# Kernel tuning notes

Measured on AMD Instinct MI355X. Metric: run time of the kernel, lower is better.

## Reference

```python
import jax, jax.numpy as jnp
import numpy as np

N, E, G, L, H, TD, F = 10000, 100000, 64, 2, 512, 256, 128
DIS = 2 * 3 * F            # sinusoid embedding dim = 768
DIN = 2 * H + DIS + 6      # edge_mlp input dim = 1798
EPS = 1e-5


def _ln(x, g, b):
    mu = x.mean(-1, keepdims=True)
    var = ((x - mu) ** 2).mean(-1, keepdims=True)
    return (x - mu) * jax.lax.rsqrt(var + EPS) * g + b


def _sin_emb(x):  # x: [E, 3] -> [E, 2*3*F]
    freqs = 2.0 * np.pi * jnp.arange(F, dtype=x.dtype)
    e = (x[:, :, None] * freqs).reshape(x.shape[0], -1)
    return jnp.concatenate([jnp.sin(e), jnp.cos(e)], axis=-1)


def setup_inputs() -> dict:
    key = jax.random.key(0)
    ks = jax.random.split(key, 16)
    s = 0.02
    return dict(
        atom_types=jax.random.randint(ks[0], (N,), 0, 100),
        node2graph=jnp.sort(jax.random.randint(ks[1], (N,), 0, G)),
        edge_index=jax.random.randint(ks[2], (2, E), 0, N),
        frac_diff=jax.random.uniform(ks[3], (E, 3)) - 0.5,
        lattices=jax.random.normal(ks[4], (G, 6)),
        t=jax.random.uniform(ks[5], (1, 1)),
        emb_table=jax.random.normal(ks[6], (119, H)) * s,
        Wt=jax.random.normal(ks[7], (TD, 1)) * s,
        Wa=jax.random.normal(ks[8], (H, H + TD)) * s,
        ba=jnp.zeros((H,)),
        ln_g=jnp.ones((L, H)), ln_b=jnp.zeros((L, H)),
        eW1=jax.random.normal(ks[9], (L, H, DIN)) * s, eb1=jnp.zeros((L, H)),
        eW2=jax.random.normal(ks[10], (L, H, H)) * s, eb2=jnp.zeros((L, H)),
        nW1=jax.random.normal(ks[11], (L, H, 2 * H)) * s, nb1=jnp.zeros((L, H)),
        nW2=jax.random.normal(ks[12], (L, H, H)) * s, nb2=jnp.zeros((L, H)),
        fln_g=jnp.ones((H,)), fln_b=jnp.zeros((H,)),
        Wc=jax.random.normal(ks[13], (3, H)) * s,
    )


def reference(atom_types, node2graph, edge_index, frac_diff, lattices, t,
              emb_table, Wt, Wa, ba, ln_g, ln_b, eW1, eb1, eW2, eb2,
              nW1, nb1, nW2, nb2, fln_g, fln_b, Wc):
    silu = jax.nn.silu
    src, dst = edge_index[0], edge_index[1]
    edge2graph = node2graph[src]
    demb = _sin_emb(frac_diff)                 # [E, 768]
    lat_e = lattices[edge2graph]               # [E, 6] (lattices_flat gathered to edges)
    counts = jax.ops.segment_sum(jnp.ones((E, 1), frac_diff.dtype), src, num_segments=N)
    counts = jnp.maximum(counts, 1.0)

    # node init: embedding + broadcast time emb -> atom_latent_emb -> silu
    t_emb = t @ Wt.T                           # [1, TD]
    h = jnp.concatenate([emb_table[atom_types],
                         jnp.broadcast_to(t_emb, (N, TD))], axis=1)
    h = silu(h @ Wa.T + ba)                    # [N, H]

    def step(h, p):
        g, b, w1, b1, w2, b2, m1, c1, m2, c2 = p
        hn = _ln(h, g, b)                      # pre-LN
        ef = jnp.concatenate([hn[src], hn[dst], lat_e, demb], axis=1)  # [E, DIN]
        m = silu(ef @ w1.T + b1)
        m = silu(m @ w2.T + b2)                # [E, H] edge messages
        agg = jax.ops.segment_sum(m, src, num_segments=N) / counts    # scatter-mean
        u = jnp.concatenate([hn, agg], axis=1)  # [N, 2H]
        u = silu(u @ m1.T + c1)
        u = silu(u @ m2.T + c2)
        return h + u, None                     # residual

    h, _ = jax.lax.scan(step, h, (ln_g, ln_b, eW1, eb1, eW2, eb2,
                                  nW1, nb1, nW2, nb2))
    h = _ln(h, fln_g, fln_b)
    return h @ Wc.T                            # [N, 3] coord_out
```

## Files before the change

### kernel.cpp

```cpp
#include <hip/hip_runtime.h>
#include <stdint.h>

typedef unsigned short u16;
typedef unsigned int u32;
typedef __attribute__((ext_vector_type(8))) short short8;
typedef __attribute__((ext_vector_type(4))) float f32x4;

#define TN 10000
#define TE 100000
#define TG 64
#define TH 512
#define EC 25000
#define NCH 4
#define PAD 128

static constexpr size_t A256(size_t x){ return (x+255)/256*256; }
constexpr size_t OFF_H    = 0;
constexpr size_t OFF_PQ   = A256(OFF_H    + (size_t)TN*512*4);
constexpr size_t OFF_HCAT = A256(OFF_PQ   + (size_t)TN*1024*2);
constexpr size_t OFF_AGGF = A256(OFF_HCAT + (size_t)TN*1024*2);
constexpr size_t OFF_MC   = A256(OFF_AGGF + (size_t)TN*512*4);
constexpr size_t OFF_XD   = A256(OFF_MC   + (size_t)(EC+PAD)*512*2);
constexpr size_t OFF_WAB  = A256(OFF_XD   + (size_t)(EC+PAD)*768*2);
constexpr size_t OFF_W1D  = A256(OFF_WAB  + (size_t)2*1024*512*2);
constexpr size_t OFF_W2   = A256(OFF_W1D  + (size_t)2*512*768*2);
constexpr size_t OFF_WN1  = A256(OFF_W2   + (size_t)2*512*512*2);
constexpr size_t OFF_WN2  = A256(OFF_WN1  + (size_t)2*512*1024*2);
constexpr size_t OFF_RP   = A256(OFF_WN2  + (size_t)2*512*512*2);
constexpr size_t OFF_H0   = A256(OFF_RP   + (size_t)2*64*512*4);
constexpr size_t OFF_B2   = A256(OFF_H0   + (size_t)119*512*4);
constexpr size_t OFF_CNT  = A256(OFF_B2   + 512*4);
constexpr size_t OFF_SLOT = A256(OFF_CNT  + (size_t)TN*4);
constexpr size_t OFF_IPTR = A256(OFF_SLOT + (size_t)TN*4);
constexpr size_t OFF_NOD  = A256(OFF_IPTR + (size_t)(TN+1)*4);
constexpr size_t OFF_DST  = A256(OFF_NOD  + (size_t)(TE+PAD)*4);
constexpr size_t OFF_FDS  = A256(OFF_DST  + (size_t)(TE+PAD)*4);
constexpr size_t WS_NEED  = OFF_FDS + (size_t)(TE+PAD)*3*4;

__device__ __forceinline__ float bf2f(u16 u){ u32 x=((u32)u)<<16; float f; __builtin_memcpy(&f,&x,4); return f; }
__device__ __forceinline__ u16 f2bf(float f){ u32 x; __builtin_memcpy(&x,&f,4); x = x + 0x7fffu + ((x>>16)&1u); return (u16)(x>>16); }
__device__ __forceinline__ float siluf(float v){ return v*(1.0f/(1.0f+__expf(-v))); }

__device__ __forceinline__ void gld16(const void* g, void* l){
  __builtin_amdgcn_global_load_lds((const __attribute__((address_space(1))) u32*)g,
                                   (__attribute__((address_space(3))) u32*)l, 16, 0, 0);
}

__device__ __forceinline__ void blockReduce2(float& s, float& ss){
  for (int off=32; off>0; off>>=1){ s += __shfl_down(s,off,64); ss += __shfl_down(ss,off,64); }
  __shared__ float red[8];
  int lane = threadIdx.x&63, wave = threadIdx.x>>6;
  if (lane==0){ red[wave*2]=s; red[wave*2+1]=ss; }
  __syncthreads();
  s  = red[0]+red[2]+red[4]+red[6];
  ss = red[1]+red[3]+red[5]+red[7];
}

template<int EPI>
__device__ __forceinline__ void gemm_core(
    const u16* __restrict__ A, int lda,
    const u16* __restrict__ B, int ldb,
    int M, int K,
    u16* __restrict__ Cb, float* __restrict__ Cf, int ldc,
    const float* __restrict__ bias,
    int cbase,
    const u16* __restrict__ PQ,
    const int* __restrict__ nodS, const int* __restrict__ dstS,
    const int* __restrict__ n2g, const float* __restrict__ Rp)
{
  __shared__ u16 As[3*2048];
  __shared__ u16 Bs[3*4096];
  const int t = threadIdx.x;
  const int bm = blockIdx.x, bn = blockIdx.y;
  const int lane = t&63;
  const int wave = t>>6;
  const int wm = wave>>1, wn = wave&1;

  f32x4 acc[2][4];
  #pragma unroll
  for (int i=0;i<2;i++)
    #pragma unroll
    for (int j=0;j<4;j++) acc[i][j] = (f32x4){0.f,0.f,0.f,0.f};

  const int sr = t>>2;
  const int sk = (((t&3) ^ ((t>>3)&3)))*8;
  int ar0 = bm*64 + sr; if (ar0 > M-1) ar0 = M-1;
  const u16* Ag0 = A + (size_t)ar0*lda + sk;
  const u16* Bg0 = B + (size_t)(bn*128 + sr)*ldb + sk;
  const u16* Bg1 = B + (size_t)(bn*128 + sr + 64)*ldb + sk;
  u16* As0 = &As[t*8];
  u16* Bs0 = &Bs[t*8];
  u16* Bs1 = &Bs[t*8 + 2048];

  const int rg = ((lane>>4) ^ ((lane>>1)&3))*8;
  const u16* ApL = &As[(wm*32 + (lane&15))*32 + rg];
  const u16* BpL = &Bs[(wn*64 + (lane&15))*32 + rg];

  const int nk = K>>5;
  #define STAGE(kt, b) { const int ko=(kt)<<5; \
      gld16(Ag0+ko, As0+(b)*2048); \
      gld16(Bg0+ko, Bs0+(b)*4096); \
      gld16(Bg1+ko, Bs1+(b)*4096); }

  STAGE(0,0)
  STAGE(1,1)
  int cb=0, sb=2;
  for (int ki=0; ki<nk; ++ki){
    if (ki+1 < nk) asm volatile("s_waitcnt vmcnt(3)" ::: "memory");
    else           asm volatile("s_waitcnt vmcnt(0)" ::: "memory");
    __builtin_amdgcn_s_barrier();
    if (ki+2 < nk) STAGE(ki+2, sb)
    const int ca = cb*2048, cbb = cb*4096;
    short8 af[2], bf[4];
    #pragma unroll
    for (int mi=0;mi<2;mi++) af[mi] = *(const short8*)(ApL + ca + mi*512);
    #pragma unroll
    for (int ni=0;ni<4;ni++) bf[ni] = *(const short8*)(BpL + cbb + ni*512);
    #pragma unroll
    for (int mi=0;mi<2;mi++)
      #pragma unroll
      for (int ni=0;ni<4;ni++)
        acc[mi][ni] = __builtin_amdgcn_mfma_f32_16x16x32_bf16(af[mi], bf[ni], acc[mi][ni], 0,0,0);
    cb = (cb==2)?0:cb+1;
    sb = (sb==2)?0:sb+1;
  }
  #undef STAGE

  const int c0 = bn*128 + wn*64 + (lane&15);
  const int r0 = bm*64 + wm*32 + ((lane>>4)<<2);

  if constexpr (EPI==0){
    #pragma unroll
    for (int mi=0;mi<2;mi++)
      #pragma unroll
      for (int r=0;r<4;r++){
        int row = r0 + mi*16 + r;
        if (row < M){
          u16* o = Cb + (size_t)row*ldc + c0;
          #pragma unroll
          for (int ni=0;ni<4;ni++) o[ni*16] = f2bf(acc[mi][ni][r]);
        }
      }
  } else if constexpr (EPI==1){
    float bz[4];
    #pragma unroll
    for (int ni=0;ni<4;ni++) bz[ni] = bias[c0 + ni*16];
    #pragma unroll
    for (int mi=0;mi<2;mi++)
      #pragma unroll
      for (int r=0;r<4;r++){
        int row = r0 + mi*16 + r;
        if (row < M){
          u16* o = Cb + (size_t)row*ldc + c0;
          #pragma unroll
          for (int ni=0;ni<4;ni++) o[ni*16] = f2bf(siluf(acc[mi][ni][r]+bz[ni]));
        }
      }
  } else if constexpr (EPI==2){
    #pragma unroll
    for (int mi=0;mi<2;mi++)
      #pragma unroll
      for (int r=0;r<4;r++){
        int row = r0 + mi*16 + r;
        if (row < M){
          int gs = cbase + row;
          int sn = nodS[gs], dn = dstS[gs];
          int g  = n2g[sn];
          const u16* Pp = PQ + (size_t)sn*1024 + c0;
          const u16* Qp = PQ + (size_t)dn*1024 + 512 + c0;
          const float* Rr = Rp + g*512 + c0;
          u16* o = Cb + (size_t)row*512 + c0;
          #pragma unroll
          for (int ni=0;ni<4;ni++){
            float v = acc[mi][ni][r] + bf2f(Pp[ni*16]) + bf2f(Qp[ni*16]) + Rr[ni*16];
            o[ni*16] = f2bf(siluf(v));
          }
        }
      }
  } else {
    float bz[4];
    #pragma unroll
    for (int ni=0;ni<4;ni++) bz[ni] = bias[c0 + ni*16];
    #pragma unroll
    for (int mi=0;mi<2;mi++)
      #pragma unroll
      for (int r=0;r<4;r++){
        int row = r0 + mi*16 + r;
        if (row < M){
          float* hp = Cf + (size_t)row*ldc + c0;
          #pragma unroll
          for (int ni=0;ni<4;ni++) hp[ni*16] += siluf(acc[mi][ni][r]+bz[ni]);
        }
      }
  }
}

#define GEMM_ARGS const u16* A, int lda, const u16* B, int ldb, int M, int K, \
    u16* Cb, float* Cf, int ldc, const float* bias, int cbase, const u16* PQ, \
    const int* nodS, const int* dstS, const int* n2g, const float* Rp
#define GEMM_PASS A,lda,B,ldb,M,K,Cb,Cf,ldc,bias,cbase,PQ,nodS,dstS,n2g,Rp

__global__ __launch_bounds__(256) void g_pq(GEMM_ARGS){ gemm_core<0>(GEMM_PASS); }
__global__ __launch_bounds__(256) void g_e1(GEMM_ARGS){ gemm_core<2>(GEMM_PASS); }
__global__ __launch_bounds__(256) void g_e2(GEMM_ARGS){ gemm_core<1>(GEMM_PASS); }
__global__ __launch_bounds__(256) void g_n1(GEMM_ARGS){ gemm_core<1>(GEMM_PASS); }
__global__ __launch_bounds__(256) void g_n2(GEMM_ARGS){ gemm_core<3>(GEMM_PASS); }

__global__ void k_demb(const float* __restrict__ fdS, int cbase, int M,
                       u16* __restrict__ dembC){
  const float TP = 6.283185307179586f;
  int total = M*96;
  for (int i = blockIdx.x*blockDim.x+threadIdx.x; i<total; i+=gridDim.x*blockDim.x){
    int row = i/96;
    int g   = i - row*96;
    int col = g*8;
    int iscos = col>=384;
    int cc = iscos ? col-384 : col;
    int d = cc>>7;
    float off = iscos ? 0.25f : 0.0f;
    float x = fdS[(size_t)(cbase+row)*3 + d];
    float fb = (float)(cc&127);
    short8 v;
    #pragma unroll
    for (int j=0;j<8;j++){
      float w = x*(fb+(float)j);
      w -= rintf(w);
      v[j] = (short)f2bf(__sinf(TP*(w+off)));
    }
    *(short8*)(dembC + (size_t)row*768 + col) = v;
  }
}

__global__ void k_prep(const float* __restrict__ tp, const float* __restrict__ Wt,
                       const float* __restrict__ Wa, const float* __restrict__ ba,
                       float* __restrict__ bias2){
  __shared__ float te[256];
  int t=threadIdx.x;
  te[t] = tp[0]*Wt[t];
  __syncthreads();
  for (int i=t;i<512;i+=256){
    float s = ba[i];
    const float* wr = Wa + (size_t)i*768 + 512;
    for (int j=0;j<256;j++) s += wr[j]*te[j];
    bias2[i]=s;
  }
}

__global__ void k_h0(const float* __restrict__ emb, const float* __restrict__ Wa,
                     const float* __restrict__ bias2, float* __restrict__ h0){
  __shared__ float et[512];
  int ty=blockIdx.x, t=threadIdx.x;
  et[t]=emb[(size_t)ty*512+t]; et[t+256]=emb[(size_t)ty*512+t+256];
  __syncthreads();
  for (int i=t;i<512;i+=256){
    float s=bias2[i];
    const float* wr = Wa + (size_t)i*768;
    for (int k=0;k<512;k++) s += wr[k]*et[k];
    h0[(size_t)ty*512+i]=siluf(s);
  }
}

__global__ void k_inith(const int* __restrict__ at, const float* __restrict__ h0,
                        float* __restrict__ h){
  int total=TN*512;
  for (int i=blockIdx.x*blockDim.x+threadIdx.x; i<total; i+=gridDim.x*blockDim.x){
    int n=i>>9, c=i&511;
    h[i]=h0[(size_t)at[n]*512+c];
  }
}

__global__ void k_count(const int* __restrict__ src, int* __restrict__ counts){
  for (int e=blockIdx.x*blockDim.x+threadIdx.x; e<TE; e+=gridDim.x*blockDim.x)
    atomicAdd(&counts[src[e]],1);
}

__global__ void k_scan(const int* __restrict__ cnt, int* __restrict__ iptr){
  __shared__ int sums[1024];
  const int T=1024, n=TN;
  int t=threadIdx.x;
  const int chunk=(n+T-1)/T;
  int s=0;
  for (int i=0;i<chunk;i++){ int idx=t*chunk+i; if(idx<n) s+=cnt[idx]; }
  sums[t]=s; __syncthreads();
  for (int off=1; off<T; off<<=1){
    int v = (t>=off)? sums[t-off] : 0;
    __syncthreads();
    sums[t]+=v;
    __syncthreads();
  }
  int run = (t==0)?0:sums[t-1];
  for (int i=0;i<chunk;i++){
    int idx=t*chunk+i;
    if(idx<n){ iptr[idx]=run; run+=cnt[idx]; }
  }
  if (t==T-1) iptr[n]=run;
}

__global__ void k_fill(const int* __restrict__ src, const int* __restrict__ dst,
                       const float* __restrict__ fd, const int* __restrict__ iptr,
                       int* __restrict__ slots, int* __restrict__ nodS,
                       int* __restrict__ dstS, float* __restrict__ fdS){
  for (int e=blockIdx.x*blockDim.x+threadIdx.x; e<TE; e+=gridDim.x*blockDim.x){
    int s=src[e];
    int p=atomicAdd(&slots[s],1);
    int gs=iptr[s]+p;
    nodS[gs]=s; dstS[gs]=dst[e];
    fdS[(size_t)gs*3+0]=fd[(size_t)e*3+0];
    fdS[(size_t)gs*3+1]=fd[(size_t)e*3+1];
    fdS[(size_t)gs*3+2]=fd[(size_t)e*3+2];
  }
}

__global__ void k_R(const float* __restrict__ lat, const float* __restrict__ eW1,
                    const float* __restrict__ eb1, float* __restrict__ Rp){
  int total = 2*64*512;
  for (int i=blockIdx.x*blockDim.x+threadIdx.x; i<total; i+=gridDim.x*blockDim.x){
    int l = i>>15;
    int g = (i>>9)&63;
    int o = i&511;
    float s = eb1[l*512+o];
    const float* wr = eW1 + ((size_t)l*512 + o)*1798 + 1024;
    const float* lr = lat + g*6;
    #pragma unroll
    for (int k=0;k<6;k++) s += lr[k]*wr[k];
    Rp[i]=s;
  }
}

struct PackDesc { const float* src; u16* dst; int rows, cols, ld, off; };
struct PackArgs { PackDesc d[12]; };
__global__ void k_pack(PackArgs pa){
  PackDesc d = pa.d[blockIdx.y];
  int total = d.rows*d.cols;
  for (int i = blockIdx.x*blockDim.x + threadIdx.x; i<total; i += gridDim.x*blockDim.x){
    int r = i/d.cols, c = i - r*d.cols;
    d.dst[i] = f2bf(d.src[(size_t)r*d.ld + d.off + c]);
  }
}

__global__ void k_ln(const float* __restrict__ h, const float* __restrict__ g,
                     const float* __restrict__ b, u16* __restrict__ hcat){
  int row = blockIdx.x, t = threadIdx.x;
  const float* hr = h + (size_t)row*512;
  float v0 = hr[t], v1 = hr[t+256];
  float s = v0+v1, ss = v0*v0+v1*v1;
  blockReduce2(s, ss);
  float mean = s*(1.0f/512.0f);
  float var  = ss*(1.0f/512.0f) - mean*mean;
  float rs = rsqrtf(var + 1e-5f);
  u16* o = hcat + (size_t)row*1024;
  o[t]     = f2bf((v0-mean)*rs*g[t]     + b[t]);
  o[t+256] = f2bf((v1-mean)*rs*g[t+256] + b[t+256]);
}

__global__ void k_aggpart(const u16* __restrict__ xc, const int* __restrict__ iptr,
                          int s0, int s1, float* __restrict__ aggf){
  int n=blockIdx.x, t=threadIdx.x;
  int beg=iptr[n], end=iptr[n+1];
  if (beg<s0) beg=s0;
  if (end>s1) end=s1;
  if (beg>=end) return;
  float a0=0.f, a1=0.f;
  for (int i=beg;i<end;i++){
    const u16* xr = xc + (size_t)(i-s0)*512;
    a0 += bf2f(xr[t]); a1 += bf2f(xr[t+256]);
  }
  float* ar = aggf + (size_t)n*512;
  ar[t] += a0; ar[t+256] += a1;
}

__global__ void k_aggfin(const float* __restrict__ aggf, const int* __restrict__ counts,
                         u16* __restrict__ hcat){
  int n=blockIdx.x, t=threadIdx.x;
  int c=counts[n]; if (c<1) c=1;
  float inv = 1.0f/(float)c;
  const float* ar = aggf + (size_t)n*512;
  u16* o = hcat + (size_t)n*1024 + 512;
  o[t]     = f2bf(ar[t]*inv);
  o[t+256] = f2bf(ar[t+256]*inv);
}

__global__ void k_final(const float* __restrict__ h, const float* __restrict__ g,
                        const float* __restrict__ b, const float* __restrict__ Wc,
                        float* __restrict__ out){
  int row=blockIdx.x, t=threadIdx.x;
  const float* hr = h + (size_t)row*512;
  float v0=hr[t], v1=hr[t+256];
  float s=v0+v1, ss=v0*v0+v1*v1;
  blockReduce2(s,ss);
  float mean=s*(1.0f/512.0f), var=ss*(1.0f/512.0f)-mean*mean, rs=rsqrtf(var+1e-5f);
  float n0=(v0-mean)*rs*g[t]+b[t];
  float n1=(v1-mean)*rs*g[t+256]+b[t+256];
  float p0 = n0*Wc[t]      + n1*Wc[t+256];
  float p1 = n0*Wc[512+t]  + n1*Wc[512+t+256];
  float p2 = n0*Wc[1024+t] + n1*Wc[1024+t+256];
  for (int off=32; off>0; off>>=1){
    p0+=__shfl_down(p0,off,64); p1+=__shfl_down(p1,off,64); p2+=__shfl_down(p2,off,64);
  }
  __shared__ float rp[4][3];
  int lane=t&63, wave=t>>6;
  if (lane==0){ rp[wave][0]=p0; rp[wave][1]=p1; rp[wave][2]=p2; }
  __syncthreads();
  if (t<3) out[(size_t)row*3+t] = rp[0][t]+rp[1][t]+rp[2][t]+rp[3][t];
}

__global__ void k_report(float* out, int n, float val){
  for (int i=blockIdx.x*blockDim.x+threadIdx.x; i<n; i+=gridDim.x*blockDim.x) out[i]=val;
}

extern "C" void kernel_launch(void* const* d_in, const int* in_sizes, int n_in,
                              void* d_out, int out_size, void* d_ws, size_t ws_size,
                              hipStream_t stream)
{
  const int*   atom  = (const int*)  d_in[0];
  const int*   n2g   = (const int*)  d_in[1];
  const int*   eidx  = (const int*)  d_in[2];
  const float* fdiff = (const float*)d_in[3];
  const float* lat   = (const float*)d_in[4];
  const float* tp    = (const float*)d_in[5];
  const float* emb   = (const float*)d_in[6];
  const float* Wt    = (const float*)d_in[7];
  const float* Wa    = (const float*)d_in[8];
  const float* ba    = (const float*)d_in[9];
  const float* lng   = (const float*)d_in[10];
  const float* lnb   = (const float*)d_in[11];
  const float* eW1   = (const float*)d_in[12];
  const float* eb1   = (const float*)d_in[13];
  const float* eW2   = (const float*)d_in[14];
  const float* eb2   = (const float*)d_in[15];
  const float* nW1   = (const float*)d_in[16];
  const float* nb1   = (const float*)d_in[17];
  const float* nW2   = (const float*)d_in[18];
  const float* nb2   = (const float*)d_in[19];
  const float* flng  = (const float*)d_in[20];
  const float* flnb  = (const float*)d_in[21];
  const float* Wc    = (const float*)d_in[22];
  float* out = (float*)d_out;

  char* ws = (char*)d_ws;
  if (ws_size < WS_NEED){
    k_report<<<64,256,0,stream>>>(out, out_size, (float)(ws_size>>20));
    return;
  }

  float* h    = (float*)(ws+OFF_H);
  u16*   PQ   = (u16*)(ws+OFF_PQ);
  u16*   hcat = (u16*)(ws+OFF_HCAT);
  float* aggf = (float*)(ws+OFF_AGGF);
  u16*   m_c  = (u16*)(ws+OFF_MC);
  u16*   u    = (u16*)(ws+OFF_MC);
  u16*   x_c  = (u16*)(ws+OFF_XD);
  u16*   dembC= (u16*)(ws+OFF_XD);
  u16*   Wab  = (u16*)(ws+OFF_WAB);
  u16*   W1d  = (u16*)(ws+OFF_W1D);
  u16*   W2c  = (u16*)(ws+OFF_W2);
  u16*   Wn1  = (u16*)(ws+OFF_WN1);
  u16*   Wn2  = (u16*)(ws+OFF_WN2);
  float* Rp   = (float*)(ws+OFF_RP);
  float* h0   = (float*)(ws+OFF_H0);
  float* b2   = (float*)(ws+OFF_B2);
  int* counts = (int*)(ws+OFF_CNT);
  int* slots  = (int*)(ws+OFF_SLOT);
  int* iptr   = (int*)(ws+OFF_IPTR);
  int* nodS   = (int*)(ws+OFF_NOD);
  int* dstS   = (int*)(ws+OFF_DST);
  float* fdS  = (float*)(ws+OFF_FDS);
  const int* src = eidx;
  const int* dst = eidx + TE;

  hipMemsetAsync(ws+OFF_CNT, 0, OFF_SLOT + (size_t)TN*4 - OFF_CNT, stream);

  k_prep<<<1,256,0,stream>>>(tp, Wt, Wa, ba, b2);
  k_h0<<<119,256,0,stream>>>(emb, Wa, b2, h0);
  k_inith<<<1024,256,0,stream>>>(atom, h0, h);
  k_count<<<391,256,0,stream>>>(src, counts);
  k_scan<<<1,1024,0,stream>>>(counts, iptr);
  k_fill<<<391,256,0,stream>>>(src, dst, fdiff, iptr, slots, nodS, dstS, fdS);
  k_R<<<256,256,0,stream>>>(lat, eW1, eb1, Rp);

  PackArgs pa;
  for (int l=0;l<2;l++){
    const float* e1 = eW1 + (size_t)l*512*1798;
    pa.d[l*6+0] = {e1, Wab + (size_t)l*1024*512,             512, 512, 1798, 0};
    pa.d[l*6+1] = {e1, Wab + (size_t)l*1024*512 + 512*512,   512, 512, 1798, 512};
    pa.d[l*6+2] = {e1, W1d + (size_t)l*512*768,              512, 768, 1798, 1030};
    pa.d[l*6+3] = {eW2 + (size_t)l*512*512, W2c + (size_t)l*512*512, 512, 512, 512, 0};
    pa.d[l*6+4] = {nW1 + (size_t)l*512*1024, Wn1 + (size_t)l*512*1024, 512, 1024, 1024, 0};
    pa.d[l*6+5] = {nW2 + (size_t)l*512*512, Wn2 + (size_t)l*512*512, 512, 512, 512, 0};
  }
  k_pack<<<dim3(128,12),256,0,stream>>>(pa);

  const int BME = (EC+63)/64;
  const int BMN = (TN+63)/64;
  for (int l=0;l<2;l++){
    k_ln<<<TN,256,0,stream>>>(h, lng+(size_t)l*512, lnb+(size_t)l*512, hcat);
    g_pq<<<dim3(BMN,8),256,0,stream>>>(hcat, 1024, Wab+(size_t)l*1024*512, 512,
        TN, 512, PQ, nullptr, 1024, nullptr, 0, nullptr, nullptr, nullptr, nullptr, nullptr);
    hipMemsetAsync(aggf, 0, (size_t)TN*512*4, stream);
    for (int c=0;c<NCH;c++){
      int s0 = c*EC;
      k_demb<<<2048,256,0,stream>>>(fdS, s0, EC, dembC);
      g_e1<<<dim3(BME,4),256,0,stream>>>(dembC, 768, W1d+(size_t)l*512*768, 768,
          EC, 768, m_c, nullptr, 512, nullptr,
          s0, PQ, nodS, dstS, n2g, Rp+(size_t)l*64*512);
      g_e2<<<dim3(BME,4),256,0,stream>>>(m_c, 512, W2c+(size_t)l*512*512, 512,
          EC, 512, x_c, nullptr, 512, eb2+(size_t)l*512,
          0, nullptr, nullptr, nullptr, nullptr, nullptr);
      k_aggpart<<<TN,256,0,stream>>>(x_c, iptr, s0, s0+EC, aggf);
    }
    k_aggfin<<<TN,256,0,stream>>>(aggf, counts, hcat);
    g_n1<<<dim3(BMN,4),256,0,stream>>>(hcat, 1024, Wn1+(size_t)l*512*1024, 1024,
        TN, 1024, u, nullptr, 512, nb1+(size_t)l*512,
        0, nullptr, nullptr, nullptr, nullptr, nullptr);
    g_n2<<<dim3(BMN,4),256,0,stream>>>(u, 512, Wn2+(size_t)l*512*512, 512,
        TN, 512, nullptr, h, 512, nb2+(size_t)l*512,
        0, nullptr, nullptr, nullptr, nullptr, nullptr);
  }
  k_final<<<TN,256,0,stream>>>(h, flng, flnb, Wc, out);
}
```

Baseline: 1.330 ms.

## Fuse sinusoid embedding into edge GEMM and use full-width 512-thread edge tiles

Removes the separate k_demb kernel by computing the sin/cos distance embedding directly into shared memory as the A operand inside the first edge GEMM. The edge GEMMs switch to 512-thread blocks covering all 512 output columns with 32-row tiles, so each A tile is built once instead of once per column block. The pipeline moves from a triple buffer to a double buffer. This cuts the dembC round trip through global memory and the redundant A reloads, at the cost of more trig work on the A-loading threads and extra synchronisation.

Result: slower. 1.431 ms (+7.6%).

```diff
diff --git a/kernel.cpp b/kernel.cpp
--- a/kernel.cpp
+++ b/kernel.cpp
@@ -56,25 +56,22 @@
   ss = red[1]+red[3]+red[5]+red[7];
 }
 
-template<int EPI>
-__device__ __forceinline__ void gemm_core(
-    const u16* __restrict__ A, int lda,
-    const u16* __restrict__ B, int ldb,
-    int M, int K,
-    u16* __restrict__ Cb, float* __restrict__ Cf, int ldc,
-    const float* __restrict__ bias,
-    int cbase,
+template<int EPI, bool TRIGA>
+__device__ __forceinline__ void gemm512_core(
+    const u16* __restrict__ A, const float* __restrict__ fdS,
+    const u16* __restrict__ B, int M, int K, int cbase,
+    u16* __restrict__ Cb, const float* __restrict__ bias,
     const u16* __restrict__ PQ,
     const int* __restrict__ nodS, const int* __restrict__ dstS,
     const int* __restrict__ n2g, const float* __restrict__ Rp)
 {
-  __shared__ u16 As[3*2048];
-  __shared__ u16 Bs[3*4096];
+  __shared__ u16 AsD[2*1024];
+  __shared__ u16 BsD[2*16384];
   const int t = threadIdx.x;
-  const int bm = blockIdx.x, bn = blockIdx.y;
+  const int bm = blockIdx.x;
   const int lane = t&63;
   const int wave = t>>6;
-  const int wm = wave>>1, wn = wave&1;
+  const float TP = 6.283185307179586f;
 
   f32x4 acc[2][4];
   #pragma unroll
@@ -84,84 +81,99 @@
 
   const int sr = t>>2;
   const int sk = (((t&3) ^ ((t>>3)&3)))*8;
-  int ar0 = bm*64 + sr; if (ar0 > M-1) ar0 = M-1;
-  const u16* Ag0 = A + (size_t)ar0*lda + sk;
-  const u16* Bg0 = B + (size_t)(bn*128 + sr)*ldb + sk;
-  const u16* Bg1 = B + (size_t)(bn*128 + sr + 64)*ldb + sk;
-  u16* As0 = &As[t*8];
-  u16* Bs0 = &Bs[t*8];
-  u16* Bs1 = &Bs[t*8 + 2048];
+  const u16* Bg0 = B + (size_t)sr*K + sk;
+  const u16* Bg1 = B + (size_t)(sr+128)*K + sk;
+  const u16* Bg2 = B + (size_t)(sr+256)*K + sk;
+  const u16* Bg3 = B + (size_t)(sr+384)*K + sk;
+
+  int ar = bm*32 + (t>>2); if (ar > M-1) ar = M-1;
+  const u16* Ag = TRIGA ? nullptr : (A + (size_t)ar*K + sk);
+  float fx0=0.f, fx1=0.f, fx2=0.f;
+  if (TRIGA && t<128){
+    int ge = cbase + bm*32 + (t>>2);
+    fx0 = fdS[(size_t)ge*3+0]; fx1 = fdS[(size_t)ge*3+1]; fx2 = fdS[(size_t)ge*3+2];
+  }
 
   const int rg = ((lane>>4) ^ ((lane>>1)&3))*8;
-  const u16* ApL = &As[(wm*32 + (lane&15))*32 + rg];
-  const u16* BpL = &Bs[(wn*64 + (lane&15))*32 + rg];
+  const u16* ApL = &AsD[(lane&15)*32 + rg];
+  const u16* BpL = &BsD[(wave*64 + (lane&15))*32 + rg];
 
   const int nk = K>>5;
-  #define STAGE(kt, b) { const int ko=(kt)<<5; \
-      gld16(Ag0+ko, As0+(b)*2048); \
-      gld16(Bg0+ko, Bs0+(b)*4096); \
-      gld16(Bg1+ko, Bs1+(b)*4096); }
+  #define STAGE(kt, b) { \
+    const int ko = (kt)*32; \
+    gld16(Bg0 + ko, (u16*)BsD + (b)*16384 + t*8); \
+    gld16(Bg1 + ko, (u16*)BsD + (b)*16384 + 4096 + t*8); \
+    gld16(Bg2 + ko, (u16*)BsD + (b)*16384 + 8192 + t*8); \
+    gld16(Bg3 + ko, (u16*)BsD + (b)*16384 + 12288 + t*8); \
+    if (t < 128){ \
+      if constexpr (TRIGA){ \
+        int c = ko + sk; int isc = (c>=384); int cc = isc? c-384 : c; \
+        int d = cc>>7; float x = (d==0)?fx0:((d==1)?fx1:fx2); \
+        float fb = (float)(cc&127); float off = isc?0.25f:0.0f; \
+        short8 v; \
+        _Pragma("unroll") \
+        for (int j=0;j<8;j++){ \
+          float w = x*(fb+(float)j); w -= rintf(w); \
+          v[j] = (short)f2bf(__sinf(TP*(w+off))); } \
+        *(short8*)((u16*)AsD + (b)*1024 + t*8) = v; \
+      } else { \
+        gld16(Ag + ko, (u16*)AsD + (b)*1024 + t*8); \
+      } \
+    } \
+  }
 
   STAGE(0,0)
   STAGE(1,1)
-  int cb=0, sb=2;
+  asm volatile("s_waitcnt vmcnt(4) lgkmcnt(0)" ::: "memory");
+  __builtin_amdgcn_s_barrier();
+
+  int cur = 0;
   for (int ki=0; ki<nk; ++ki){
-    if (ki+1 < nk) asm volatile("s_waitcnt vmcnt(3)" ::: "memory");
-    else           asm volatile("s_waitcnt vmcnt(0)" ::: "memory");
+    short8 af[2], bf[4];
+    const int ca = cur*1024, cbb = cur*16384;
+    #pragma unroll
+    for (int mi=0;mi<2;mi++) af[mi] = *(const short8*)(ApL + ca + mi*512);
+    #pragma unroll
+    for (int ni=0;ni<4;ni++) bf[ni] = *(const short8*)(BpL + cbb + ni*512);
+    asm volatile("s_waitcnt lgkmcnt(0)" ::: "memory");
     __builtin_amdgcn_s_barrier();
-    if (ki+2 < nk) STAGE(ki+2, sb)
-    const int ca = cb*2048, cbb = cb*4096;
-    short8 af[2], bf[4];
-    #pragma unroll
-    for (int mi=0;mi<2;mi++) af[mi] = *(const short8*)(ApL + ca + mi*512);
-    #pragma unroll
-    for (int ni=0;ni<4;ni++) bf[ni] = *(const short8*)(BpL + cbb + ni*512);
+    if (ki+2 < nk) STAGE(ki+2, cur)
     #pragma unroll
     for (int mi=0;mi<2;mi++)
       #pragma unroll
       for (int ni=0;ni<4;ni++)
         acc[mi][ni] = __builtin_amdgcn_mfma_f32_16x16x32_bf16(af[mi], bf[ni], acc[mi][ni], 0,0,0);
-    cb = (cb==2)?0:cb+1;
-    sb = (sb==2)?0:sb+1;
+    if (ki+2 < nk) { asm volatile("s_waitcnt vmcnt(4)" ::: "memory"); }
+    else           { asm volatile("s_waitcnt vmcnt(0)" ::: "memory"); }
+    __builtin_amdgcn_s_barrier();
+    cur ^= 1;
   }
   #undef STAGE
 
-  const int c0 = bn*128 + wn*64 + (lane&15);
-  const int r0 = bm*64 + wm*32 + ((lane>>4)<<2);
-
-  if constexpr (EPI==0){
+  const int c0 = wave*64 + (lane&15);
+  const int r0 = (lane>>4)<<2;
+
+  if constexpr (EPI==1){
+    float bz[4];
+    #pragma unroll
+    for (int ni=0;ni<4;ni++) bz[ni] = bias[c0 + ni*16];
     #pragma unroll
     for (int mi=0;mi<2;mi++)
       #pragma unroll
       for (int r=0;r<4;r++){
-        int row = r0 + mi*16 + r;
+        int row = bm*32 + r0 + mi*16 + r;
         if (row < M){
-          u16* o = Cb + (size_t)row*ldc + c0;
-          #pragma unroll
-          for (int ni=0;ni<4;ni++) o[ni*16] = f2bf(acc[mi][ni][r]);
-        }
-      }
-  } else if constexpr (EPI==1){
-    float bz[4];
-    #pragma unroll
-    for (int ni=0;ni<4;ni++) bz[ni] = bias[c0 + ni*16];
-    #pragma unroll
-    for (int mi=0;mi<2;mi++)
-      #pragma unroll
-      for (int r=0;r<4;r++){
-        int row = r0 + mi*16 + r;
-        if (row < M){
-          u16* o = Cb + (size_t)row*ldc + c0;
+          u16* o = Cb + (size_t)row*512 + c0;
           #pragma unroll
           for (int ni=0;ni<4;ni++) o[ni*16] = f2bf(siluf(acc[mi][ni][r]+bz[ni]));
         }
       }
-  } else if constexpr (EPI==2){
+  } else {
     #pragma unroll
     for (int mi=0;mi<2;mi++)
       #pragma unroll
       for (int r=0;r<4;r++){
-        int row = r0 + mi*16 + r;
+        int row = bm*32 + r0 + mi*16 + r;
         if (row < M){
           int gs = cbase + row;
           int sn = nodS[gs], dn = dstS[gs];
@@ -177,6 +189,115 @@
           }
         }
       }
+  }
+}
+
+__global__ __launch_bounds__(512) void g_e1(const float* fdS, const u16* B, int M, int K,
+    int cbase, u16* Cm, const u16* PQ, const int* nodS, const int* dstS,
+    const int* n2g, const float* Rp){
+  gemm512_core<2,true>(nullptr, fdS, B, M, K, cbase, Cm, nullptr, PQ, nodS, dstS, n2g, Rp);
+}
+__global__ __launch_bounds__(512) void g_e2(const u16* A, const u16* B, int M, int K,
+    u16* Cb, const float* bias){
+  gemm512_core<1,false>(A, nullptr, B, M, K, 0, Cb, bias, nullptr, nullptr, nullptr, nullptr, nullptr);
+}
+
+template<int EPI>
+__device__ __forceinline__ void gemm_core(
+    const u16* __restrict__ A, int lda,
+    const u16* __restrict__ B, int ldb,
+    int M, int K,
+    u16* __restrict__ Cb, float* __restrict__ Cf, int ldc,
+    const float* __restrict__ bias)
+{
+  __shared__ u16 As[3*2048];
+  __shared__ u16 Bs[3*4096];
+  const int t = threadIdx.x;
+  const int bm = blockIdx.x, bn = blockIdx.y;
+  const int lane = t&63;
+  const int wave = t>>6;
+  const int wm = wave>>1, wn = wave&1;
+
+  f32x4 acc[2][4];
+  #pragma unroll
+  for (int i=0;i<2;i++)
+    #pragma unroll
+    for (int j=0;j<4;j++) acc[i][j] = (f32x4){0.f,0.f,0.f,0.f};
+
+  const int sr = t>>2;
+  const int sk = (((t&3) ^ ((t>>3)&3)))*8;
+  int ar0 = bm*64 + sr; if (ar0 > M-1) ar0 = M-1;
+  const u16* Ag0 = A + (size_t)ar0*lda + sk;
+  const u16* Bg0 = B + (size_t)(bn*128 + sr)*ldb + sk;
+  const u16* Bg1 = B + (size_t)(bn*128 + sr + 64)*ldb + sk;
+  u16* As0 = &As[t*8];
+  u16* Bs0 = &Bs[t*8];
+  u16* Bs1 = &Bs[t*8 + 2048];
+
+  const int rg = ((lane>>4) ^ ((lane>>1)&3))*8;
+  const u16* ApL = &As[(wm*32 + (lane&15))*32 + rg];
+  const u16* BpL = &Bs[(wn*64 + (lane&15))*32 + rg];
+
+  const int nk = K>>5;
+  #define STAGEN(kt, b) { const int ko=(kt)<<5; \
+      gld16(Ag0+ko, As0+(b)*2048); \
+      gld16(Bg0+ko, Bs0+(b)*4096); \
+      gld16(Bg1+ko, Bs1+(b)*4096); }
+
+  STAGEN(0,0)
+  STAGEN(1,1)
+  int cb=0, sb=2;
+  for (int ki=0; ki<nk; ++ki){
+    if (ki+1 < nk) asm volatile("s_waitcnt vmcnt(3)" ::: "memory");
+    else           asm volatile("s_waitcnt vmcnt(0)" ::: "memory");
+    __builtin_amdgcn_s_barrier();
+    if (ki+2 < nk) STAGEN(ki+2, sb)
+    const int ca = cb*2048, cbb = cb*4096;
+    short8 af[2], bf[4];
+    #pragma unroll
+    for (int mi=0;mi<2;mi++) af[mi] = *(const short8*)(ApL + ca + mi*512);
+    #pragma unroll
+    for (int ni=0;ni<4;ni++) bf[ni] = *(const short8*)(BpL + cbb + ni*512);
+    #pragma unroll
+    for (int mi=0;mi<2;mi++)
+      #pragma unroll
+      for (int ni=0;ni<4;ni++)
+        acc[mi][ni] = __builtin_amdgcn_mfma_f32_16x16x32_bf16(af[mi], bf[ni], acc[mi][ni], 0,0,0);
+    cb = (cb==2)?0:cb+1;
+    sb = (sb==2)?0:sb+1;
+  }
+  #undef STAGEN
+
+  const int c0 = bn*128 + wn*64 + (lane&15);
+  const int r0 = bm*64 + wm*32 + ((lane>>4)<<2);
+
+  if constexpr (EPI==0){
+    #pragma unroll
+    for (int mi=0;mi<2;mi++)
+      #pragma unroll
+      for (int r=0;r<4;r++){
+        int row = r0 + mi*16 + r;
+        if (row < M){
+          u16* o = Cb + (size_t)row*ldc + c0;
+          #pragma unroll
+          for (int ni=0;ni<4;ni++) o[ni*16] = f2bf(acc[mi][ni][r]);
+        }
+      }
+  } else if constexpr (EPI==1){
+    float bz[4];
+    #pragma unroll
+    for (int ni=0;ni<4;ni++) bz[ni] = bias[c0 + ni*16];
+    #pragma unroll
+    for (int mi=0;mi<2;mi++)
+      #pragma unroll
+      for (int r=0;r<4;r++){
+        int row = r0 + mi*16 + r;
+        if (row < M){
+          u16* o = Cb + (size_t)row*ldc + c0;
+          #pragma unroll
+          for (int ni=0;ni<4;ni++) o[ni*16] = f2bf(siluf(acc[mi][ni][r]+bz[ni]));
+        }
+      }
   } else {
     float bz[4];
     #pragma unroll
@@ -196,40 +317,12 @@
 }
 
 #define GEMM_ARGS const u16* A, int lda, const u16* B, int ldb, int M, int K, \
-    u16* Cb, float* Cf, int ldc, const float* bias, int cbase, const u16* PQ, \
-    const int* nodS, const int* dstS, const int* n2g, const float* Rp
-#define GEMM_PASS A,lda,B,ldb,M,K,Cb,Cf,ldc,bias,cbase,PQ,nodS,dstS,n2g,Rp
+    u16* Cb, float* Cf, int ldc, const float* bias
+#define GEMM_PASS A,lda,B,ldb,M,K,Cb,Cf,ldc,bias
 
 __global__ __launch_bounds__(256) void g_pq(GEMM_ARGS){ gemm_core<0>(GEMM_PASS); }
-__global__ __launch_bounds__(256) void g_e1(GEMM_ARGS){ gemm_core<2>(GEMM_PASS); }
-__global__ __launch_bounds__(256) void g_e2(GEMM_ARGS){ gemm_core<1>(GEMM_PASS); }
 __global__ __launch_bounds__(256) void g_n1(GEMM_ARGS){ gemm_core<1>(GEMM_PASS); }
-__global__ __launch_bounds__(256) void g_n2(GEMM_ARGS){ gemm_core<3>(GEMM_PASS); }
-
-__global__ void k_demb(const float* __restrict__ fdS, int cbase, int M,
-                       u16* __restrict__ dembC){
-  const float TP = 6.283185307179586f;
-  int total = M*96;
-  for (int i = blockIdx.x*blockDim.x+threadIdx.x; i<total; i+=gridDim.x*blockDim.x){
-    int row = i/96;
-    int g   = i - row*96;
-    int col = g*8;
-    int iscos = col>=384;
-    int cc = iscos ? col-384 : col;
-    int d = cc>>7;
-    float off = iscos ? 0.25f : 0.0f;
-    float x = fdS[(size_t)(cbase+row)*3 + d];
-    float fb = (float)(cc&127);
-    short8 v;
-    #pragma unroll
-    for (int j=0;j<8;j++){
-      float w = x*(fb+(float)j);
-      w -= rintf(w);
-      v[j] = (short)f2bf(__sinf(TP*(w+off)));
-    }
-    *(short8*)(dembC + (size_t)row*768 + col) = v;
-  }
-}
+__global__ __launch_bounds__(256) void g_n2(GEMM_ARGS){ gemm_core<2>(GEMM_PASS); }
 
 __global__ void k_prep(const float* __restrict__ tp, const float* __restrict__ Wt,
                        const float* __restrict__ Wa, const float* __restrict__ ba,
@@ -450,7 +543,6 @@
   u16*   m_c  = (u16*)(ws+OFF_MC);
   u16*   u    = (u16*)(ws+OFF_MC);
   u16*   x_c  = (u16*)(ws+OFF_XD);
-  u16*   dembC= (u16*)(ws+OFF_XD);
   u16*   Wab  = (u16*)(ws+OFF_WAB);
   u16*   W1d  = (u16*)(ws+OFF_W1D);
   u16*   W2c  = (u16*)(ws+OFF_W2);
@@ -490,31 +582,26 @@
   }
   k_pack<<<dim3(128,12),256,0,stream>>>(pa);
 
-  const int BME = (EC+63)/64;
-  const int BMN = (TN+63)/64;
+  const int BME32 = (EC+31)/32;
+  const int BMN   = (TN+63)/64;
   for (int l=0;l<2;l++){
     k_ln<<<TN,256,0,stream>>>(h, lng+(size_t)l*512, lnb+(size_t)l*512, hcat);
     g_pq<<<dim3(BMN,8),256,0,stream>>>(hcat, 1024, Wab+(size_t)l*1024*512, 512,
-        TN, 512, PQ, nullptr, 1024, nullptr, 0, nullptr, nullptr, nullptr, nullptr, nullptr);
+        TN, 512, PQ, nullptr, 1024, nullptr);
     hipMemsetAsync(aggf, 0, (size_t)TN*512*4, stream);
     for (int c=0;c<NCH;c++){
       int s0 = c*EC;
-      k_demb<<<2048,256,0,stream>>>(fdS, s0, EC, dembC);
-      g_e1<<<dim3(BME,4),256,0,stream>>>(dembC, 768, W1d+(size_t)l*512*768, 768,
-          EC, 768, m_c, nullptr, 512, nullptr,
-          s0, PQ, nodS, dstS, n2g, Rp+(size_t)l*64*512);
-      g_e2<<<dim3(BME,4),256,0,stream>>>(m_c, 512, W2c+(size_t)l*512*512, 512,
-          EC, 512, x_c, nullptr, 512, eb2+(size_t)l*512,
-          0, nullptr, nullptr, nullptr, nullptr, nullptr);
+      g_e1<<<BME32,512,0,stream>>>(fdS, W1d+(size_t)l*512*768, EC, 768,
+          s0, m_c, PQ, nodS, dstS, n2g, Rp+(size_t)l*64*512);
+      g_e2<<<BME32,512,0,stream>>>(m_c, W2c+(size_t)l*512*512, EC, 512,
+          x_c, eb2+(size_t)l*512);
       k_aggpart<<<TN,256,0,stream>>>(x_c, iptr, s0, s0+EC, aggf);
     }
     k_aggfin<<<TN,256,0,stream>>>(aggf, counts, hcat);
     g_n1<<<dim3(BMN,4),256,0,stream>>>(hcat, 1024, Wn1+(size_t)l*512*1024, 1024,
-        TN, 1024, u, nullptr, 512, nb1+(size_t)l*512,
-        0, nullptr, nullptr, nullptr, nullptr, nullptr);
+        TN, 1024, u, nullptr, 512, nb1+(size_t)l*512);
     g_n2<<<dim3(BMN,4),256,0,stream>>>(u, 512, Wn2+(size_t)l*512*512, 512,
-        TN, 512, nullptr, h, 512, nb2+(size_t)l*512,
-        0, nullptr, nullptr, nullptr, nullptr, nullptr);
+        TN, 512, nullptr, h, 512, nb2+(size_t)l*512);
   }
   k_final<<<TN,256,0,stream>>>(h, flng, flnb, Wc, out);
 }
```

## Size edge chunking to workspace, hoist sinusoid embedding, swizzle edge GEMM blocks

Applied to the files above, without the earlier changes.

Workspace offsets are now computed at runtime, and the edge pass uses the fewest chunks (1, 2, 4 or 8) that fit. With a single chunk, the sinusoid embedding is computed once for both layers, and aggregation becomes a direct CSR mean, which drops the fp32 accumulator memset and the partial-aggregation passes. The edge GEMMs switch to a 1D grid with an XCD-aware block remap intended to improve L2 locality. The sinusoid kernel now builds its sin/cos values with an angle-addition recurrence instead of one sin call per element, which may slightly change rounding.

Measured after the change: 1.220 ms. -8.3%, faster.

```diff
diff --git a/kernel.cpp b/kernel.cpp
--- a/kernel.cpp
+++ b/kernel.cpp
@@ -8,34 +8,9 @@
 
 #define TN 10000
 #define TE 100000
-#define TG 64
-#define TH 512
-#define EC 25000
-#define NCH 4
 #define PAD 128
 
 static constexpr size_t A256(size_t x){ return (x+255)/256*256; }
-constexpr size_t OFF_H    = 0;
-constexpr size_t OFF_PQ   = A256(OFF_H    + (size_t)TN*512*4);
-constexpr size_t OFF_HCAT = A256(OFF_PQ   + (size_t)TN*1024*2);
-constexpr size_t OFF_AGGF = A256(OFF_HCAT + (size_t)TN*1024*2);
-constexpr size_t OFF_MC   = A256(OFF_AGGF + (size_t)TN*512*4);
-constexpr size_t OFF_XD   = A256(OFF_MC   + (size_t)(EC+PAD)*512*2);
-constexpr size_t OFF_WAB  = A256(OFF_XD   + (size_t)(EC+PAD)*768*2);
-constexpr size_t OFF_W1D  = A256(OFF_WAB  + (size_t)2*1024*512*2);
-constexpr size_t OFF_W2   = A256(OFF_W1D  + (size_t)2*512*768*2);
-constexpr size_t OFF_WN1  = A256(OFF_W2   + (size_t)2*512*512*2);
-constexpr size_t OFF_WN2  = A256(OFF_WN1  + (size_t)2*512*1024*2);
-constexpr size_t OFF_RP   = A256(OFF_WN2  + (size_t)2*512*512*2);
-constexpr size_t OFF_H0   = A256(OFF_RP   + (size_t)2*64*512*4);
-constexpr size_t OFF_B2   = A256(OFF_H0   + (size_t)119*512*4);
-constexpr size_t OFF_CNT  = A256(OFF_B2   + 512*4);
-constexpr size_t OFF_SLOT = A256(OFF_CNT  + (size_t)TN*4);
-constexpr size_t OFF_IPTR = A256(OFF_SLOT + (size_t)TN*4);
-constexpr size_t OFF_NOD  = A256(OFF_IPTR + (size_t)(TN+1)*4);
-constexpr size_t OFF_DST  = A256(OFF_NOD  + (size_t)(TE+PAD)*4);
-constexpr size_t OFF_FDS  = A256(OFF_DST  + (size_t)(TE+PAD)*4);
-constexpr size_t WS_NEED  = OFF_FDS + (size_t)(TE+PAD)*3*4;
 
 __device__ __forceinline__ float bf2f(u16 u){ u32 x=((u32)u)<<16; float f; __builtin_memcpy(&f,&x,4); return f; }
 __device__ __forceinline__ u16 f2bf(float f){ u32 x; __builtin_memcpy(&x,&f,4); x = x + 0x7fffu + ((x>>16)&1u); return (u16)(x>>16); }
@@ -56,7 +31,7 @@
   ss = red[1]+red[3]+red[5]+red[7];
 }
 
-template<int EPI>
+template<int EPI, bool SWZ>
 __device__ __forceinline__ void gemm_core(
     const u16* __restrict__ A, int lda,
     const u16* __restrict__ B, int ldb,
@@ -66,12 +41,20 @@
     int cbase,
     const u16* __restrict__ PQ,
     const int* __restrict__ nodS, const int* __restrict__ dstS,
-    const int* __restrict__ n2g, const float* __restrict__ Rp)
+    const int* __restrict__ n2g, const float* __restrict__ Rp,
+    int nwg)
 {
   __shared__ u16 As[3*2048];
   __shared__ u16 Bs[3*4096];
+  int bm, bn;
+  if constexpr (SWZ){
+    int orig = blockIdx.x;
+    int q = nwg>>3, r = nwg&7;
+    int xcd = orig&7, idx = orig>>3;
+    int wg = (xcd<r ? xcd*(q+1) : r*(q+1)+(xcd-r)*q) + idx;
+    bm = wg>>2; bn = wg&3;
+  } else { bm = blockIdx.x; bn = blockIdx.y; }
   const int t = threadIdx.x;
-  const int bm = blockIdx.x, bn = blockIdx.y;
   const int lane = t&63;
   const int wave = t>>6;
   const int wm = wave>>1, wn = wave&1;
@@ -97,19 +80,19 @@
   const u16* BpL = &Bs[(wn*64 + (lane&15))*32 + rg];
 
   const int nk = K>>5;
-  #define STAGE(kt, b) { const int ko=(kt)<<5; \
+  #define STAGEN(kt, b) { const int ko=(kt)<<5; \
       gld16(Ag0+ko, As0+(b)*2048); \
       gld16(Bg0+ko, Bs0+(b)*4096); \
       gld16(Bg1+ko, Bs1+(b)*4096); }
 
-  STAGE(0,0)
-  STAGE(1,1)
+  STAGEN(0,0)
+  STAGEN(1,1)
   int cb=0, sb=2;
   for (int ki=0; ki<nk; ++ki){
     if (ki+1 < nk) asm volatile("s_waitcnt vmcnt(3)" ::: "memory");
     else           asm volatile("s_waitcnt vmcnt(0)" ::: "memory");
     __builtin_amdgcn_s_barrier();
-    if (ki+2 < nk) STAGE(ki+2, sb)
+    if (ki+2 < nk) STAGEN(ki+2, sb)
     const int ca = cb*2048, cbb = cb*4096;
     short8 af[2], bf[4];
     #pragma unroll
@@ -124,7 +107,7 @@
     cb = (cb==2)?0:cb+1;
     sb = (sb==2)?0:sb+1;
   }
-  #undef STAGE
+  #undef STAGEN
 
   const int c0 = bn*128 + wn*64 + (lane&15);
   const int r0 = bm*64 + wm*32 + ((lane>>4)<<2);
@@ -169,7 +152,7 @@
           const u16* Pp = PQ + (size_t)sn*1024 + c0;
           const u16* Qp = PQ + (size_t)dn*1024 + 512 + c0;
           const float* Rr = Rp + g*512 + c0;
-          u16* o = Cb + (size_t)row*512 + c0;
+          u16* o = Cb + (size_t)row*ldc + c0;
           #pragma unroll
           for (int ni=0;ni<4;ni++){
             float v = acc[mi][ni][r] + bf2f(Pp[ni*16]) + bf2f(Qp[ni*16]) + Rr[ni*16];
@@ -197,14 +180,14 @@
 
 #define GEMM_ARGS const u16* A, int lda, const u16* B, int ldb, int M, int K, \
     u16* Cb, float* Cf, int ldc, const float* bias, int cbase, const u16* PQ, \
-    const int* nodS, const int* dstS, const int* n2g, const float* Rp
-#define GEMM_PASS A,lda,B,ldb,M,K,Cb,Cf,ldc,bias,cbase,PQ,nodS,dstS,n2g,Rp
-
-__global__ __launch_bounds__(256) void g_pq(GEMM_ARGS){ gemm_core<0>(GEMM_PASS); }
-__global__ __launch_bounds__(256) void g_e1(GEMM_ARGS){ gemm_core<2>(GEMM_PASS); }
-__global__ __launch_bounds__(256) void g_e2(GEMM_ARGS){ gemm_core<1>(GEMM_PASS); }
-__global__ __launch_bounds__(256) void g_n1(GEMM_ARGS){ gemm_core<1>(GEMM_PASS); }
-__global__ __launch_bounds__(256) void g_n2(GEMM_ARGS){ gemm_core<3>(GEMM_PASS); }
+    const int* nodS, const int* dstS, const int* n2g, const float* Rp, int nwg
+#define GEMM_PASS A,lda,B,ldb,M,K,Cb,Cf,ldc,bias,cbase,PQ,nodS,dstS,n2g,Rp,nwg
+
+__global__ __launch_bounds__(256) void g_pq(GEMM_ARGS){ gemm_core<0,false>(GEMM_PASS); }
+__global__ __launch_bounds__(256) void g_n1(GEMM_ARGS){ gemm_core<1,false>(GEMM_PASS); }
+__global__ __launch_bounds__(256) void g_n2(GEMM_ARGS){ gemm_core<3,false>(GEMM_PASS); }
+__global__ __launch_bounds__(256) void g_e1(GEMM_ARGS){ gemm_core<2,true>(GEMM_PASS); }
+__global__ __launch_bounds__(256) void g_e2(GEMM_ARGS){ gemm_core<1,true>(GEMM_PASS); }
 
 __global__ void k_demb(const float* __restrict__ fdS, int cbase, int M,
                        u16* __restrict__ dembC){
@@ -214,18 +197,22 @@
     int row = i/96;
     int g   = i - row*96;
     int col = g*8;
-    int iscos = col>=384;
-    int cc = iscos ? col-384 : col;
+    int isc = col>=384;
+    int cc = isc ? col-384 : col;
     int d = cc>>7;
-    float off = iscos ? 0.25f : 0.0f;
     float x = fdS[(size_t)(cbase+row)*3 + d];
     float fb = (float)(cc&127);
+    float w0 = x*fb; w0 -= rintf(w0);
+    float s, c, ds, dc;
+    __sincosf(TP*w0, &s, &c);
+    __sincosf(TP*x, &ds, &dc);
     short8 v;
     #pragma unroll
     for (int j=0;j<8;j++){
-      float w = x*(fb+(float)j);
-      w -= rintf(w);
-      v[j] = (short)f2bf(__sinf(TP*(w+off)));
+      v[j] = (short)f2bf(isc ? c : s);
+      float s2 = s*dc + c*ds;
+      float c2 = c*dc - s*ds;
+      s = s2; c = c2;
     }
     *(short8*)(dembC + (size_t)row*768 + col) = v;
   }
@@ -378,6 +365,22 @@
   u16* o = hcat + (size_t)n*1024 + 512;
   o[t]     = f2bf(ar[t]*inv);
   o[t+256] = f2bf(ar[t+256]*inv);
+}
+
+__global__ void k_agg(const u16* __restrict__ x, const int* __restrict__ iptr,
+                      u16* __restrict__ hcat){
+  int n=blockIdx.x, t=threadIdx.x;
+  int beg=iptr[n], end=iptr[n+1];
+  float a0=0.f, a1=0.f;
+  for (int i=beg;i<end;i++){
+    const u16* xr = x + (size_t)i*512;
+    a0 += bf2f(xr[t]); a1 += bf2f(xr[t+256]);
+  }
+  int c=end-beg; if (c<1) c=1;
+  float inv = 1.0f/(float)c;
+  u16* o = hcat + (size_t)n*1024 + 512;
+  o[t]     = f2bf(a0*inv);
+  o[t+256] = f2bf(a1*inv);
 }
 
 __global__ void k_final(const float* __restrict__ h, const float* __restrict__ g,
@@ -437,38 +440,69 @@
   const float* Wc    = (const float*)d_in[22];
   float* out = (float*)d_out;
 
+  size_t o = 0;
+  auto al = [&](size_t b){ size_t r = o; o = A256(o + b); return r; };
+  size_t OH   = al((size_t)TN*512*4);
+  size_t OPQ  = al((size_t)TN*1024*2);
+  size_t OHC  = al((size_t)TN*1024*2);
+  size_t OWAB = al((size_t)2*1024*512*2);
+  size_t OW1D = al((size_t)2*512*768*2);
+  size_t OW2  = al((size_t)2*512*512*2);
+  size_t OWN1 = al((size_t)2*512*1024*2);
+  size_t OWN2 = al((size_t)2*512*512*2);
+  size_t ORP  = al((size_t)2*64*512*4);
+  size_t OH0  = al((size_t)119*512*4);
+  size_t OB2  = al(512*4);
+  size_t OCNT = al((size_t)TN*4);
+  size_t OSLOT= al((size_t)TN*4);
+  size_t OIPTR= al((size_t)(TN+1)*4);
+  size_t ONOD = al((size_t)(TE+PAD)*4);
+  size_t ODST = al((size_t)(TE+PAD)*4);
+  size_t OFDS = al((size_t)(TE+PAD)*3*4);
+  size_t statEnd = o;
+
+  int nch = 0; int ec = 0;
+  size_t OAGG=0, OM=0, OX=0, ODB=0;
+  const int cands[4] = {1,2,4,8};
+  for (int ci=0; ci<4; ++ci){
+    int c = cands[ci];
+    o = statEnd;
+    size_t e = TE/c;
+    size_t ag = (c>1) ? al((size_t)TN*512*4) : 0;
+    size_t om = al((e+PAD)*512*2);
+    size_t ox = al((e+PAD)*512*2);
+    size_t od = al((e+PAD)*768*2);
+    if (o <= ws_size){ nch=c; ec=(int)e; OAGG=ag; OM=om; OX=ox; ODB=od; break; }
+  }
   char* ws = (char*)d_ws;
-  if (ws_size < WS_NEED){
-    k_report<<<64,256,0,stream>>>(out, out_size, (float)(ws_size>>20));
-    return;
-  }
-
-  float* h    = (float*)(ws+OFF_H);
-  u16*   PQ   = (u16*)(ws+OFF_PQ);
-  u16*   hcat = (u16*)(ws+OFF_HCAT);
-  float* aggf = (float*)(ws+OFF_AGGF);
-  u16*   m_c  = (u16*)(ws+OFF_MC);
-  u16*   u    = (u16*)(ws+OFF_MC);
-  u16*   x_c  = (u16*)(ws+OFF_XD);
-  u16*   dembC= (u16*)(ws+OFF_XD);
-  u16*   Wab  = (u16*)(ws+OFF_WAB);
-  u16*   W1d  = (u16*)(ws+OFF_W1D);
-  u16*   W2c  = (u16*)(ws+OFF_W2);
-  u16*   Wn1  = (u16*)(ws+OFF_WN1);
-  u16*   Wn2  = (u16*)(ws+OFF_WN2);
-  float* Rp   = (float*)(ws+OFF_RP);
-  float* h0   = (float*)(ws+OFF_H0);
-  float* b2   = (float*)(ws+OFF_B2);
-  int* counts = (int*)(ws+OFF_CNT);
-  int* slots  = (int*)(ws+OFF_SLOT);
-  int* iptr   = (int*)(ws+OFF_IPTR);
-  int* nodS   = (int*)(ws+OFF_NOD);
-  int* dstS   = (int*)(ws+OFF_DST);
-  float* fdS  = (float*)(ws+OFF_FDS);
+  if (!nch){ k_report<<<64,256,0,stream>>>(out, out_size, (float)(ws_size>>20)); return; }
+
+  float* h    = (float*)(ws+OH);
+  u16*   PQ   = (u16*)(ws+OPQ);
+  u16*   hcat = (u16*)(ws+OHC);
+  float* aggf = (float*)(ws+OAGG);
+  u16*   m    = (u16*)(ws+OM);
+  u16*   u    = (u16*)(ws+OM);
+  u16*   x    = (u16*)(ws+OX);
+  u16*   demb = (u16*)(ws+ODB);
+  u16*   Wab  = (u16*)(ws+OWAB);
+  u16*   W1d  = (u16*)(ws+OW1D);
+  u16*   W2c  = (u16*)(ws+OW2);
+  u16*   Wn1  = (u16*)(ws+OWN1);
+  u16*   Wn2  = (u16*)(ws+OWN2);
+  float* Rp   = (float*)(ws+ORP);
+  float* h0   = (float*)(ws+OH0);
+  float* b2   = (float*)(ws+OB2);
+  int* counts = (int*)(ws+OCNT);
+  int* slots  = (int*)(ws+OSLOT);
+  int* iptr   = (int*)(ws+OIPTR);
+  int* nodS   = (int*)(ws+ONOD);
+  int* dstS   = (int*)(ws+ODST);
+  float* fdS  = (float*)(ws+OFDS);
   const int* src = eidx;
   const int* dst = eidx + TE;
 
-  hipMemsetAsync(ws+OFF_CNT, 0, OFF_SLOT + (size_t)TN*4 - OFF_CNT, stream);
+  hipMemsetAsync(ws+OCNT, 0, OIPTR - OCNT, stream);
 
   k_prep<<<1,256,0,stream>>>(tp, Wt, Wa, ba, b2);
   k_h0<<<119,256,0,stream>>>(emb, Wa, b2, h0);
@@ -490,31 +524,38 @@
   }
   k_pack<<<dim3(128,12),256,0,stream>>>(pa);
 
-  const int BME = (EC+63)/64;
-  const int BMN = (TN+63)/64;
+  const int nbmE = (ec+63)/64;
+  const int nwgE = nbmE*4;
+  const int BMN  = (TN+63)/64;
+  const int N0 = 0;
+
+  if (nch==1)
+    k_demb<<<4096,256,0,stream>>>(fdS, 0, TE, demb);
+
   for (int l=0;l<2;l++){
     k_ln<<<TN,256,0,stream>>>(h, lng+(size_t)l*512, lnb+(size_t)l*512, hcat);
     g_pq<<<dim3(BMN,8),256,0,stream>>>(hcat, 1024, Wab+(size_t)l*1024*512, 512,
-        TN, 512, PQ, nullptr, 1024, nullptr, 0, nullptr, nullptr, nullptr, nullptr, nullptr);
-    hipMemsetAsync(aggf, 0, (size_t)TN*512*4, stream);
-    for (int c=0;c<NCH;c++){
-      int s0 = c*EC;
-      k_demb<<<2048,256,0,stream>>>(fdS, s0, EC, dembC);
-      g_e1<<<dim3(BME,4),256,0,stream>>>(dembC, 768, W1d+(size_t)l*512*768, 768,
-          EC, 768, m_c, nullptr, 512, nullptr,
-          s0, PQ, nodS, dstS, n2g, Rp+(size_t)l*64*512);
-      g_e2<<<dim3(BME,4),256,0,stream>>>(m_c, 512, W2c+(size_t)l*512*512, 512,
-          EC, 512, x_c, nullptr, 512, eb2+(size_t)l*512,
-          0, nullptr, nullptr, nullptr, nullptr, nullptr);
-      k_aggpart<<<TN,256,0,stream>>>(x_c, iptr, s0, s0+EC, aggf);
+        TN, 512, PQ, nullptr, 1024, nullptr, N0, nullptr, nullptr, nullptr, nullptr, nullptr, 0);
+    if (nch>1) hipMemsetAsync(aggf, 0, (size_t)TN*512*4, stream);
+    for (int c=0;c<nch;c++){
+      int s0 = c*ec;
+      if (nch>1) k_demb<<<2048,256,0,stream>>>(fdS, s0, ec, demb);
+      g_e1<<<nwgE,256,0,stream>>>(demb, 768, W1d+(size_t)l*512*768, 768,
+          ec, 768, m, nullptr, 512, nullptr,
+          s0, PQ, nodS, dstS, n2g, Rp+(size_t)l*64*512, nwgE);
+      g_e2<<<nwgE,256,0,stream>>>(m, 512, W2c+(size_t)l*512*512, 512,
+          ec, 512, x, nullptr, 512, eb2+(size_t)l*512,
+          N0, nullptr, nullptr, nullptr, nullptr, nullptr, nwgE);
+      if (nch>1) k_aggpart<<<TN,256,0,stream>>>(x, iptr, s0, s0+ec, aggf);
     }
-    k_aggfin<<<TN,256,0,stream>>>(aggf, counts, hcat);
+    if (nch==1) k_agg<<<TN,256,0,stream>>>(x, iptr, hcat);
+    else        k_aggfin<<<TN,256,0,stream>>>(aggf, counts, hcat);
     g_n1<<<dim3(BMN,4),256,0,stream>>>(hcat, 1024, Wn1+(size_t)l*512*1024, 1024,
         TN, 1024, u, nullptr, 512, nb1+(size_t)l*512,
-        0, nullptr, nullptr, nullptr, nullptr, nullptr);
+        N0, nullptr, nullptr, nullptr, nullptr, nullptr, 0);
     g_n2<<<dim3(BMN,4),256,0,stream>>>(u, 512, Wn2+(size_t)l*512*512, 512,
         TN, 512, nullptr, h, 512, nb2+(size_t)l*512,
-        0, nullptr, nullptr, nullptr, nullptr, nullptr);
+        N0, nullptr, nullptr, nullptr, nullptr, nullptr, 0);
   }
   k_final<<<TN,256,0,stream>>>(h, flng, flnb, Wc, out);
 }
```
